# Kernel tuning notes

Hardware: AMD Instinct MI355X
Metric: run time of the kernel (lower is better)

Reference implementation:

```python
import jax, jax.numpy as jnp
import numpy as np
from jax.scipy.special import erf, erfinv

N_OBS = 8192   # number of observations
N_LOC = 2048   # number of spatial locations (q)


def setup_inputs() -> dict:
    key = jax.random.key(0)
    k1, k2, k3, k4 = jax.random.split(key, 4)
    # random 2-D coordinates -> symmetric pairwise squared-distance matrix (zero diag)
    coords = jax.random.uniform(k1, (N_LOC, 2), dtype=jnp.float32) * 10.0
    dist_matrix = jnp.sum((coords[:, None, :] - coords[None, :, :]) ** 2, axis=-1)  # [q,q]
    Z_idx = jax.random.randint(k2, (N_OBS,), 0, N_LOC)                              # location id per obs
    y_true = jax.random.normal(k3, (N_OBS, 1), dtype=jnp.float32)
    y_pred = jax.random.normal(k4, (N_OBS, 1), dtype=jnp.float32) * 0.5
    return {
        "y_true": y_true,
        "y_pred": y_pred,
        "Z_idx": Z_idx,
        "dist_matrix": dist_matrix,
        "sig2e": jnp.array([1.0], dtype=jnp.float32),
        "sig2bs": jnp.array([0.5], dtype=jnp.float32),
        "lengthscale": jnp.array([2.0], dtype=jnp.float32),
    }


def _inverse_gaussian_cdf(u):
    # tf.math.erfinv(2*clip(u,1e-5,1-1e-5)-1) * sqrt(2)
    return erfinv(2.0 * jnp.clip(u, 1e-5, 1.0 - 1e-5) - 1.0) * jnp.sqrt(2.0)


def reference(y_true, y_pred, Z_idx, dist_matrix, sig2e, sig2bs, lengthscale):
    N = y_true.shape[0]
    q = dist_matrix.shape[0]
    dt = y_true.dtype
    # getD: exponential distance kernel over locations  D = sig2b * exp(-M / (2*ell))
    D = sig2bs[0] * jnp.exp(-dist_matrix / (2.0 * lengthscale[0]))          # [q,q]
    # getZ: dense one-hot design matrix (sparse.to_dense of SparseTensor of ones)
    Z = jax.nn.one_hot(Z_idx, q, dtype=dt)                                   # [N,q]
    # V_batch: V = Z D Z' + sig2e * I
    V = Z @ (D @ Z.T) + sig2e[0] * jnp.eye(N, dtype=dt)                      # [N,N]
    sd = jnp.sqrt(jnp.diagonal(V))                                           # sd_sqrt_V
    R = V / (sd[:, None] * sd[None, :])                                      # correlation matrix
    # Gaussian marginal: sig2 = sig2e + sig2b (diag of V)
    sig2 = sig2e[0] + sig2bs[0]
    resid = y_true - y_pred                                                  # [N,1]
    # distribution.cdf_batch: standard normal CDF of resid / sqrt(sig2)
    u = 0.5 * (erf(resid / jnp.sqrt(2.0 * sig2)) + 1.0)
    m = _inverse_gaussian_cdf(u)                                             # [N,1]
    # distribution.sum_log_pdf_batch: sum of Gaussian log-pdf
    sum_log_pdf = jnp.sum(-0.5 * jnp.log(2.0 * jnp.pi * sig2) - resid ** 2 / (2.0 * sig2))
    # solve + logdet via a single Cholesky of the correlation matrix
    L = jnp.linalg.cholesky(R)
    V_inv_m = jax.scipy.linalg.cho_solve((L, True), m)                       # R^{-1} m
    logdet = 2.0 * jnp.sum(jnp.log(jnp.diagonal(L)))                         # logdet(V) - 2*sum(log sd)
    mV_invm = m.T @ V_inv_m                                                  # [1,1]
    mtm = m.T @ m                                                            # [1,1]
    total_loss = 0.5 * logdet + 0.5 * mV_invm - 0.5 * mtm + 0.5 * sum_log_pdf
    return total_loss  # [1,1]
```

## Files before the change

### kernel.cpp

```cpp
#include <hip/hip_runtime.h>
#include <math.h>

#define Q 2048
#define NOBS 8192

__device__ __forceinline__ float rl(float v, int l) {
  return __int_as_float(__builtin_amdgcn_readlane(__float_as_int(v), l));
}

__device__ __forceinline__ float block_sum256(float v, volatile float* red) {
  int tid = threadIdx.x;
#pragma unroll
  for (int o = 32; o > 0; o >>= 1) v += __shfl_down(v, o);
  __syncthreads();
  if ((tid & 63) == 0) red[tid >> 6] = v;
  __syncthreads();
  return red[0] + red[1] + red[2] + red[3];
}

__device__ __forceinline__ float chol64_reg(float rr[64], int lane) {
  float dv = 1.0f;
#pragma unroll
  for (int j = 0; j < 64; ++j) {
    float vjj = rl(rr[j], j);
    float invd = rsqrtf(vjj);
    float lij = rr[j] * invd;
    rr[j] = lij;
    if (lane == j) dv = lij;
#pragma unroll
    for (int k = j + 1; k < 64; ++k) rr[k] -= lij * rl(lij, k);
  }
  return dv;
}

__device__ __forceinline__ void wait_flag(int* f, int target) {
  while (__hip_atomic_load(f, __ATOMIC_RELAXED, __HIP_MEMORY_SCOPE_AGENT) <
         target)
    __builtin_amdgcn_s_sleep(8);
}

__global__ __launch_bounds__(256) void obs_kernel(
    const float* __restrict__ yt, const float* __restrict__ yp,
    const int* __restrict__ zidx, const float* __restrict__ s2e_p,
    const float* __restrict__ s2b_p, float* __restrict__ t,
    int* __restrict__ cnt, float* __restrict__ scal) {
  __shared__ float red[4];
  int i = blockIdx.x * 256 + threadIdx.x;
  float s2e = s2e_p[0], s2b = s2b_p[0];
  float sig2 = s2e + s2b;
  float r = yt[i] - yp[i];
  float e = erff(r * rsqrtf(2.0f * sig2));
  float u = 0.5f * (e + 1.0f);
  u = fminf(fmaxf(u, 1e-5f), 1.0f - 1e-5f);
  float m = erfinvf(2.0f * u - 1.0f) * 1.4142135623730951f;
  float slp = -0.5f * logf(2.0f * 3.14159265358979f * sig2) - r * r / (2.0f * sig2);
  int z = zidx[i];
  atomicAdd(&t[z], m);
  atomicAdd(&cnt[z], 1);
  float s1 = block_sum256(slp, red);
  float s2 = block_sum256(m * m, red);
  if (threadIdx.x == 0) {
    atomicAdd(&scal[0], s1);
    atomicAdd(&scal[1], s2);
  }
}

__global__ __launch_bounds__(256) void build_mv(
    const float* __restrict__ dist, const float* __restrict__ s2e_p,
    const float* __restrict__ s2b_p, const float* __restrict__ ell_p,
    const int* __restrict__ cnt, const float* __restrict__ t,
    float* __restrict__ G, float* __restrict__ z, float* __restrict__ scal) {
  __shared__ float red[4];
  int j = blockIdx.x;
  float s2e = s2e_p[0], s2b = s2b_p[0], ell = ell_p[0];
  float sig2 = s2e + s2b;
  float ratio = s2b / sig2;
  float diag = s2e / sig2;
  float inv2ell = 1.0f / (2.0f * ell);
  float cj = (float)cnt[j];
  const float* drow = dist + (size_t)j * Q;
  float* grow = G + (size_t)j * Q;
  float s = 0.0f;
  for (int k = threadIdx.x; k < Q; k += 256) {
    float e = expf(-drow[k] * inv2ell);
    s += e * t[k];
    float g = sqrtf(cj * (float)cnt[k]) * (ratio * e);
    if (j == k) g += diag;
    grow[k] = g;
  }
  float tot = block_sum256(s, red);
  if (threadIdx.x == 0) {
    float wj = ratio * tot;
    z[j] = sqrtf(cj) * wj;
    atomicAdd(&scal[2], t[j] * wj);
  }
}

__global__ __launch_bounds__(64, 1) void potrf_first(
    const float* __restrict__ G, float* __restrict__ dsA,
    float* __restrict__ z, float* __restrict__ scal) {
  int lane = threadIdx.x;
  float rr[64];
  const float* row = G + (size_t)lane * Q;
#pragma unroll
  for (int k4 = 0; k4 < 16; ++k4) {
    float4 v = *(const float4*)(row + k4 * 4);
    rr[k4 * 4 + 0] = v.x; rr[k4 * 4 + 1] = v.y;
    rr[k4 * 4 + 2] = v.z; rr[k4 * 4 + 3] = v.w;
  }
  float dv = chol64_reg(rr, lane);
#pragma unroll
  for (int k4 = 0; k4 < 16; ++k4) {
    float4 st;
    st.x = rr[k4 * 4 + 0]; st.y = rr[k4 * 4 + 1];
    st.z = rr[k4 * 4 + 2]; st.w = rr[k4 * 4 + 3];
    *(float4*)(dsA + lane * 64 + k4 * 4) = st;
  }
  float lg = logf(dv);
#pragma unroll
  for (int o = 32; o > 0; o >>= 1) lg += __shfl_down(lg, o);
  if (lane == 0) atomicAdd(&scal[3], lg);
  float a = z[lane];
  float myinv = 1.0f / dv;
#pragma unroll
  for (int p = 0; p < 64; ++p) {
    float xp = rl(a, p) * rl(myinv, p);
    if (lane > p) a -= xp * rr[p];
  }
  z[lane] = a * myinv;
}

__global__ __launch_bounds__(256, 2) void step_kernel(
    float* __restrict__ G, float* __restrict__ z, float* __restrict__ scal,
    const float* __restrict__ dsR, float* __restrict__ dsW,
    int* __restrict__ flags, int j0, int ntri, int n64, int T, int mode) {
  __shared__ __align__(16) float smem[2 * 64 * 68];
  __shared__ float z1s[64];
  __shared__ float z2s[64];
  float* shA = smem;
  float* shB = smem + 64 * 68;
  int tid = threadIdx.x, bx = blockIdx.x;
  int lane = tid & 63, wv = tid >> 6;
  int s1 = (j0 >> 6) + 1;
  int D0 = j0 + 64;
  int ztop = ntri + n64 - 1;

  if (mode == 1 || (mode == 0 && bx >= ztop)) {
    int t = (mode == 1) ? bx : bx - ztop;
#pragma unroll
    for (int it = 0; it < 4; ++it) {
      int idx = it * 256 + tid;
      int r = idx >> 4, c = (idx & 15) * 4;
      float4 v = *(const float4*)(dsR + r * 64 + c);
      shA[r * 65 + c + 0] = v.x; shA[r * 65 + c + 1] = v.y;
      shA[r * 65 + c + 2] = v.z; shA[r * 65 + c + 3] = v.w;
    }
    __syncthreads();
    int rbase = D0 + t * 16 + wv * 4;
    float* g0 = G + (size_t)(rbase + 0) * Q + j0;
    float* g1 = G + (size_t)(rbase + 1) * Q + j0;
    float* g2 = G + (size_t)(rbase + 2) * Q + j0;
    float* g3 = G + (size_t)(rbase + 3) * Q + j0;
    float a0 = g0[lane], a1 = g1[lane], a2 = g2[lane], a3 = g3[lane];
    float myinv = 1.0f / shA[lane * 65 + lane];
#pragma unroll
    for (int p = 0; p < 64; ++p) {
      float ip = rl(myinv, p);
      float x0 = rl(a0, p) * ip;
      float x1 = rl(a1, p) * ip;
      float x2 = rl(a2, p) * ip;
      float x3 = rl(a3, p) * ip;
      float lv = shA[lane * 65 + p];
      if (lane > p) {
        a0 -= x0 * lv; a1 -= x1 * lv; a2 -= x2 * lv; a3 -= x3 * lv;
      }
    }
    g0[lane] = a0 * myinv; g1[lane] = a1 * myinv;
    g2[lane] = a2 * myinv; g3[lane] = a3 * myinv;
    __syncthreads();
    if (tid == 0) {
      __builtin_amdgcn_fence(__ATOMIC_RELEASE, "agent");
      __hip_atomic_fetch_add(&flags[s1 + (t >> 2)], 1, __ATOMIC_RELAXED,
                             __HIP_MEMORY_SCOPE_AGENT);
    }
    return;
  }

  if (bx == 0) {
    if (tid == 0) {
      wait_flag(&flags[s1], T);
      __builtin_amdgcn_fence(__ATOMIC_ACQUIRE, "agent");
    }
    __syncthreads();
    if (tid < 64) z1s[tid] = z[j0 + tid];
#pragma unroll
    for (int it = 0; it < 4; ++it) {
      int idx = it * 256 + tid;
      int r2 = idx >> 4, c4 = (idx & 15) * 4;
      float4 v = *(const float4*)(G + (size_t)(D0 + r2) * Q + j0 + c4);
      shA[(c4 + 0) * 68 + r2] = v.x; shA[(c4 + 1) * 68 + r2] = v.y;
      shA[(c4 + 2) * 68 + r2] = v.z; shA[(c4 + 3) * 68 + r2] = v.w;
    }
    __syncthreads();
    int tx = tid & 15, ty = tid >> 4;
    float acc[4][4] = {{0.f}};
    for (int p = 0; p < 64; ++p) {
      float4 a4 = *(const float4*)&shA[p * 68 + ty * 4];
      float4 b4 = *(const float4*)&shA[p * 68 + tx * 4];
      float av[4] = {a4.x, a4.y, a4.z, a4.w};
      float bv[4] = {b4.x, b4.y, b4.z, b4.w};
#pragma unroll
      for (int i = 0; i < 4; ++i)
#pragma unroll
        for (int jj = 0; jj < 4; ++jj) acc[i][jj] += av[i] * bv[jj];
    }
    {
      int rw = tid >> 2, part = tid & 3;
      float ssum = 0.f;
      for (int p = part; p < 64; p += 4) ssum += shA[p * 68 + rw] * z1s[p];
      ssum += __shfl_down(ssum, 2);
      ssum += __shfl_down(ssum, 1);
      if (part == 0) z2s[rw] = z[D0 + rw] - ssum;
    }
#pragma unroll
    for (int i = 0; i < 4; ++i) {
      const float* gp = G + (size_t)(D0 + ty * 4 + i) * Q + D0 + tx * 4;
      float4 g = *(const float4*)gp;
      float4 o;
      o.x = g.x - acc[i][0]; o.y = g.y - acc[i][1];
      o.z = g.z - acc[i][2]; o.w = g.w - acc[i][3];
      *(float4*)&shB[(ty * 4 + i) * 68 + tx * 4] = o;
    }
    __syncthreads();
    if (tid < 64) {
      float rr[64];
#pragma unroll
      for (int k4 = 0; k4 < 16; ++k4) {
        float4 v = *(const float4*)&shB[lane * 68 + k4 * 4];
        rr[k4 * 4 + 0] = v.x; rr[k4 * 4 + 1] = v.y;
        rr[k4 * 4 + 2] = v.z; rr[k4 * 4 + 3] = v.w;
      }
      __builtin_amdgcn_s_setprio(1);
      float dv = chol64_reg(rr, lane);
      __builtin_amdgcn_s_setprio(0);
#pragma unroll
      for (int k4 = 0; k4 < 16; ++k4) {
        float4 st;
        st.x = rr[k4 * 4 + 0]; st.y = rr[k4 * 4 + 1];
        st.z = rr[k4 * 4 + 2]; st.w = rr[k4 * 4 + 3];
        *(float4*)(dsW + lane * 64 + k4 * 4) = st;
      }
      float lg = logf(dv);
#pragma unroll
      for (int o = 32; o > 0; o >>= 1) lg += __shfl_down(lg, o);
      if (lane == 0) atomicAdd(&scal[3], lg);
      float a = z2s[lane];
      float myinv = 1.0f / dv;
#pragma unroll
      for (int p = 0; p < 64; ++p) {
        float xp = rl(a, p) * rl(myinv, p);
        if (lane > p) a -= xp * rr[p];
      }
      z[D0 + lane] = a * myinv;
    }
    return;
  }

  if (bx < ntri) {
    int job = bx;
    int bi = (int)((sqrtf(8.0f * (float)job + 1.0f) - 1.0f) * 0.5f);
    while ((bi + 1) * (bi + 2) / 2 <= job) ++bi;
    while (bi * (bi + 1) / 2 > job) --bi;
    int bk = job - bi * (bi + 1) / 2;
    if (tid == 0) {
      wait_flag(&flags[s1 + bi], T);
      if (bk != bi) wait_flag(&flags[s1 + bk], T);
      __builtin_amdgcn_fence(__ATOMIC_ACQUIRE, "agent");
    }
    __syncthreads();
    int R0 = D0 + bi * 64, C0 = D0 + bk * 64;
    bool sym = (bi == bk);
#pragma unroll
    for (int it = 0; it < 4; ++it) {
      int idx = it * 256 + tid;
      int r = idx >> 4, c4 = (idx & 15) * 4;
      float4 v = *(const float4*)(G + (size_t)(R0 + r) * Q + j0 + c4);
      shA[(c4 + 0) * 68 + r] = v.x; shA[(c4 + 1) * 68 + r] = v.y;
      shA[(c4 + 2) * 68 + r] = v.z; shA[(c4 + 3) * 68 + r] = v.w;
      if (!sym) {
        float4 u = *(const float4*)(G + (size_t)(C0 + r) * Q + j0 + c4);
        shB[(c4 + 0) * 68 + r] = u.x; shB[(c4 + 1) * 68 + r] = u.y;
        shB[(c4 + 2) * 68 + r] = u.z; shB[(c4 + 3) * 68 + r] = u.w;
      }
    }
    __syncthreads();
    const float* sB = sym ? shA : shB;
    int tx = tid & 15, ty = tid >> 4;
    float acc[4][4] = {{0.f}};
    for (int p = 0; p < 64; ++p) {
      float4 a4 = *(const float4*)&shA[p * 68 + ty * 4];
      float4 b4 = *(const float4*)&sB[p * 68 + tx * 4];
      float av[4] = {a4.x, a4.y, a4.z, a4.w};
      float bv[4] = {b4.x, b4.y, b4.z, b4.w};
#pragma unroll
      for (int i = 0; i < 4; ++i)
#pragma unroll
        for (int jj = 0; jj < 4; ++jj) acc[i][jj] += av[i] * bv[jj];
    }
#pragma unroll
    for (int i = 0; i < 4; ++i) {
      float* gp = G + (size_t)(R0 + ty * 4 + i) * Q + C0 + tx * 4;
      float4 g = *(const float4*)gp;
      g.x -= acc[i][0]; g.y -= acc[i][1];
      g.z -= acc[i][2]; g.w -= acc[i][3];
      *(float4*)gp = g;
    }
    return;
  }

  {
    int bk = bx - ntri + 1;
    if (tid == 0) {
      wait_flag(&flags[s1 + bk], T);
      __builtin_amdgcn_fence(__ATOMIC_ACQUIRE, "agent");
    }
    __syncthreads();
    if (tid < 64) z1s[tid] = z[j0 + tid];
    __syncthreads();
    int C0 = D0 + bk * 64;
    int rw = tid >> 2, part = tid & 3;
    const float* Lr = G + (size_t)(C0 + rw) * Q + j0;
    float ssum = 0.f;
    for (int p = part; p < 64; p += 4) ssum += Lr[p] * z1s[p];
    ssum += __shfl_down(ssum, 2);
    ssum += __shfl_down(ssum, 1);
    if (part == 0) z[C0 + rw] -= ssum;
  }
}

__global__ __launch_bounds__(256) void final_assemble(
    const float* __restrict__ z, const float* __restrict__ scal,
    const float* __restrict__ s2e_p, const float* __restrict__ s2b_p,
    float* __restrict__ out) {
  __shared__ float red[4];
  int tid = threadIdx.x;
  float bv = 0.f;
  for (int i = tid; i < Q; i += 256) {
    float zi = z[i];
    bv += zi * zi;
  }
  float bvs = block_sum256(bv, red);
  if (tid == 0) {
    float s2e = s2e_p[0], s2b = s2b_p[0];
    float sig2 = s2e + s2b;
    float c = s2e / sig2;
    float slp = scal[0], mtm = scal[1];
    float tw = scal[2], sl = scal[3];
    float tty = (tw - bvs) / c;
    float mrm = (mtm - tty) / c;
    float logdetR = (float)(NOBS - Q) * logf(c) + 2.0f * sl;
    out[0] = 0.5f * logdetR + 0.5f * mrm - 0.5f * mtm + 0.5f * slp;
  }
}

extern "C" void kernel_launch(void* const* d_in, const int* in_sizes, int n_in,
                              void* d_out, int out_size, void* d_ws, size_t ws_size,
                              hipStream_t stream) {
  const float* yt   = (const float*)d_in[0];
  const float* yp   = (const float*)d_in[1];
  const int*   zidx = (const int*)d_in[2];
  const float* dist = (const float*)d_in[3];
  const float* s2e  = (const float*)d_in[4];
  const float* s2b  = (const float*)d_in[5];
  const float* ell  = (const float*)d_in[6];

  float* ws   = (float*)d_ws;
  float* G    = ws;
  float* z    = ws + (size_t)Q * Q;
  float* t    = z + Q;
  int*   cntv = (int*)(t + Q);
  float* scal = t + 2 * Q;
  int*   flags = (int*)(scal + 8);
  float* dsA  = scal + 8 + 64;
  float* dsB  = dsA + 4096;

  hipMemsetAsync(t, 0, (2 * Q + 8 + 64) * sizeof(float), stream);

  obs_kernel<<<NOBS / 256, 256, 0, stream>>>(yt, yp, zidx, s2e, s2b, t, cntv, scal);
  build_mv<<<Q, 256, 0, stream>>>(dist, s2e, s2b, ell, cntv, t, G, z, scal);

  potrf_first<<<1, 64, 0, stream>>>(G, dsA, z, scal);

  for (int s = 0; s < 31; ++s) {
    int n64 = 31 - s;
    int ntri = n64 * (n64 + 1) / 2;
    int j0 = s * 64;
    int T = 4 * (s + 1);
    float* dsR = (s & 1) ? dsB : dsA;
    float* dsW = (s & 1) ? dsA : dsB;
    int gfull = ntri + 5 * n64 - 1;
    if (gfull <= 512) {
      step_kernel<<<gfull, 256, 0, stream>>>(G, z, scal, dsR, dsW, flags,
                                             j0, ntri, n64, T, 0);
    } else {
      step_kernel<<<4 * n64, 256, 0, stream>>>(G, z, scal, dsR, dsW, flags,
                                               j0, ntri, n64, T, 1);
      step_kernel<<<ntri + n64 - 1, 256, 0, stream>>>(G, z, scal, dsR, dsW,
                                                      flags, j0, ntri, n64, T, 2);
    }
  }

  final_assemble<<<1, 256, 0, stream>>>(z, scal, s2e, s2b, (float*)d_out);
}
```

Baseline: 1.038 ms.

## Replace flag-synchronized Cholesky steps with redundant per-block panel factorization

Result: slower. 1.099 ms (+5.9%).

```diff
diff --git a/kernel.cpp b/kernel.cpp
--- a/kernel.cpp
+++ b/kernel.cpp
@@ -31,12 +31,6 @@
     for (int k = j + 1; k < 64; ++k) rr[k] -= lij * rl(lij, k);
   }
   return dv;
-}
-
-__device__ __forceinline__ void wait_flag(int* f, int target) {
-  while (__hip_atomic_load(f, __ATOMIC_RELAXED, __HIP_MEMORY_SCOPE_AGENT) <
-         target)
-    __builtin_amdgcn_s_sleep(8);
 }
 
 __global__ __launch_bounds__(256) void obs_kernel(
@@ -96,189 +90,178 @@
   }
 }
 
-__global__ __launch_bounds__(64, 1) void potrf_first(
-    const float* __restrict__ G, float* __restrict__ dsA,
-    float* __restrict__ z, float* __restrict__ scal) {
-  int lane = threadIdx.x;
-  float rr[64];
-  const float* row = G + (size_t)lane * Q;
-#pragma unroll
-  for (int k4 = 0; k4 < 16; ++k4) {
-    float4 v = *(const float4*)(row + k4 * 4);
-    rr[k4 * 4 + 0] = v.x; rr[k4 * 4 + 1] = v.y;
-    rr[k4 * 4 + 2] = v.z; rr[k4 * 4 + 3] = v.w;
-  }
-  float dv = chol64_reg(rr, lane);
-#pragma unroll
-  for (int k4 = 0; k4 < 16; ++k4) {
-    float4 st;
-    st.x = rr[k4 * 4 + 0]; st.y = rr[k4 * 4 + 1];
-    st.z = rr[k4 * 4 + 2]; st.w = rr[k4 * 4 + 3];
-    *(float4*)(dsA + lane * 64 + k4 * 4) = st;
-  }
-  float lg = logf(dv);
-#pragma unroll
-  for (int o = 32; o > 0; o >>= 1) lg += __shfl_down(lg, o);
-  if (lane == 0) atomicAdd(&scal[3], lg);
-  float a = z[lane];
-  float myinv = 1.0f / dv;
-#pragma unroll
-  for (int p = 0; p < 64; ++p) {
-    float xp = rl(a, p) * rl(myinv, p);
-    if (lane > p) a -= xp * rr[p];
-  }
-  z[lane] = a * myinv;
-}
-
-__global__ __launch_bounds__(256, 2) void step_kernel(
+__global__ __launch_bounds__(256, 1) void estep(
     float* __restrict__ G, float* __restrict__ z, float* __restrict__ scal,
-    const float* __restrict__ dsR, float* __restrict__ dsW,
-    int* __restrict__ flags, int j0, int ntri, int n64, int T, int mode) {
-  __shared__ __align__(16) float smem[2 * 64 * 68];
+    int j1, int m, int ntile) {
+  __shared__ __align__(16) float shA[64 * 68];
+  __shared__ __align__(16) float shB[64 * 68];
+  __shared__ __align__(16) float LT[64 * 64];
+  __shared__ float invDs[64];
   __shared__ float z1s[64];
   __shared__ float z2s[64];
-  float* shA = smem;
-  float* shB = smem + 64 * 68;
   int tid = threadIdx.x, bx = blockIdx.x;
-  int lane = tid & 63, wv = tid >> 6;
-  int s1 = (j0 >> 6) + 1;
-  int D0 = j0 + 64;
-  int ztop = ntri + n64 - 1;
-
-  if (mode == 1 || (mode == 0 && bx >= ztop)) {
-    int t = (mode == 1) ? bx : bx - ztop;
-#pragma unroll
-    for (int it = 0; it < 4; ++it) {
-      int idx = it * 256 + tid;
-      int r = idx >> 4, c = (idx & 15) * 4;
-      float4 v = *(const float4*)(dsR + r * 64 + c);
-      shA[r * 65 + c + 0] = v.x; shA[r * 65 + c + 1] = v.y;
-      shA[r * 65 + c + 2] = v.z; shA[r * 65 + c + 3] = v.w;
-    }
-    __syncthreads();
-    int rbase = D0 + t * 16 + wv * 4;
-    float* g0 = G + (size_t)(rbase + 0) * Q + j0;
-    float* g1 = G + (size_t)(rbase + 1) * Q + j0;
-    float* g2 = G + (size_t)(rbase + 2) * Q + j0;
-    float* g3 = G + (size_t)(rbase + 3) * Q + j0;
-    float a0 = g0[lane], a1 = g1[lane], a2 = g2[lane], a3 = g3[lane];
-    float myinv = 1.0f / shA[lane * 65 + lane];
-#pragma unroll
-    for (int p = 0; p < 64; ++p) {
-      float ip = rl(myinv, p);
-      float x0 = rl(a0, p) * ip;
-      float x1 = rl(a1, p) * ip;
-      float x2 = rl(a2, p) * ip;
-      float x3 = rl(a3, p) * ip;
-      float lv = shA[lane * 65 + p];
-      if (lane > p) {
-        a0 -= x0 * lv; a1 -= x1 * lv; a2 -= x2 * lv; a3 -= x3 * lv;
-      }
-    }
-    g0[lane] = a0 * myinv; g1[lane] = a1 * myinv;
-    g2[lane] = a2 * myinv; g3[lane] = a3 * myinv;
-    __syncthreads();
-    if (tid == 0) {
-      __builtin_amdgcn_fence(__ATOMIC_RELEASE, "agent");
-      __hip_atomic_fetch_add(&flags[s1 + (t >> 2)], 1, __ATOMIC_RELAXED,
-                             __HIP_MEMORY_SCOPE_AGENT);
-    }
-    return;
-  }
-
-  if (bx == 0) {
-    if (tid == 0) {
-      wait_flag(&flags[s1], T);
-      __builtin_amdgcn_fence(__ATOMIC_ACQUIRE, "agent");
-    }
-    __syncthreads();
-    if (tid < 64) z1s[tid] = z[j0 + tid];
-#pragma unroll
-    for (int it = 0; it < 4; ++it) {
-      int idx = it * 256 + tid;
-      int r2 = idx >> 4, c4 = (idx & 15) * 4;
-      float4 v = *(const float4*)(G + (size_t)(D0 + r2) * Q + j0 + c4);
-      shA[(c4 + 0) * 68 + r2] = v.x; shA[(c4 + 1) * 68 + r2] = v.y;
-      shA[(c4 + 2) * 68 + r2] = v.z; shA[(c4 + 3) * 68 + r2] = v.w;
-    }
-    __syncthreads();
-    int tx = tid & 15, ty = tid >> 4;
-    float acc[4][4] = {{0.f}};
-    for (int p = 0; p < 64; ++p) {
-      float4 a4 = *(const float4*)&shA[p * 68 + ty * 4];
-      float4 b4 = *(const float4*)&shA[p * 68 + tx * 4];
-      float av[4] = {a4.x, a4.y, a4.z, a4.w};
-      float bv[4] = {b4.x, b4.y, b4.z, b4.w};
-#pragma unroll
-      for (int i = 0; i < 4; ++i)
-#pragma unroll
-        for (int jj = 0; jj < 4; ++jj) acc[i][jj] += av[i] * bv[jj];
-    }
-    {
-      int rw = tid >> 2, part = tid & 3;
-      float ssum = 0.f;
-      for (int p = part; p < 64; p += 4) ssum += shA[p * 68 + rw] * z1s[p];
-      ssum += __shfl_down(ssum, 2);
-      ssum += __shfl_down(ssum, 1);
-      if (part == 0) z2s[rw] = z[D0 + rw] - ssum;
-    }
-#pragma unroll
-    for (int i = 0; i < 4; ++i) {
-      const float* gp = G + (size_t)(D0 + ty * 4 + i) * Q + D0 + tx * 4;
-      float4 g = *(const float4*)gp;
-      float4 o;
-      o.x = g.x - acc[i][0]; o.y = g.y - acc[i][1];
-      o.z = g.z - acc[i][2]; o.w = g.w - acc[i][3];
-      *(float4*)&shB[(ty * 4 + i) * 68 + tx * 4] = o;
-    }
-    __syncthreads();
+  int lane = tid & 63;
+  int j0 = j1 - 64;
+  int tx = tid & 15, ty = tid >> 4;
+
+  if (bx <= m) {
+    bool isdiag = (bx == 0);
+    int R0 = j1 + bx * 64;
+
+    if (j1 > 0) {
+#pragma unroll
+      for (int it = 0; it < 4; ++it) {
+        int idx = it * 256 + tid;
+        int r = idx >> 4, c4 = (idx & 15) * 4;
+        float4 v = *(const float4*)(G + (size_t)(j1 + r) * Q + j0 + c4);
+        shA[(c4 + 0) * 68 + r] = v.x; shA[(c4 + 1) * 68 + r] = v.y;
+        shA[(c4 + 2) * 68 + r] = v.z; shA[(c4 + 3) * 68 + r] = v.w;
+        if (!isdiag) {
+          float4 u = *(const float4*)(G + (size_t)(R0 + r) * Q + j0 + c4);
+          shB[(c4 + 0) * 68 + r] = u.x; shB[(c4 + 1) * 68 + r] = u.y;
+          shB[(c4 + 2) * 68 + r] = u.z; shB[(c4 + 3) * 68 + r] = u.w;
+        }
+      }
+      if (isdiag && tid < 64) z1s[tid] = z[j0 + tid];
+      __syncthreads();
+
+      float acc1[4][4] = {{0.f}};
+      float acc2[4][4] = {{0.f}};
+#pragma unroll 8
+      for (int p = 0; p < 64; ++p) {
+        float4 a4 = *(const float4*)&shA[p * 68 + ty * 4];
+        float4 b4 = *(const float4*)&shA[p * 68 + tx * 4];
+        float av[4] = {a4.x, a4.y, a4.z, a4.w};
+        float bv[4] = {b4.x, b4.y, b4.z, b4.w};
+#pragma unroll
+        for (int i = 0; i < 4; ++i)
+#pragma unroll
+          for (int jj = 0; jj < 4; ++jj) acc2[i][jj] += av[i] * bv[jj];
+        if (!isdiag) {
+          float4 c4v = *(const float4*)&shB[p * 68 + ty * 4];
+          float cv[4] = {c4v.x, c4v.y, c4v.z, c4v.w};
+#pragma unroll
+          for (int i = 0; i < 4; ++i)
+#pragma unroll
+            for (int jj = 0; jj < 4; ++jj) acc1[i][jj] += cv[i] * bv[jj];
+        }
+      }
+      if (isdiag) {
+        int rw = tid >> 2, part = tid & 3;
+        float ssum = 0.f;
+        for (int p = part; p < 64; p += 4) ssum += shA[p * 68 + rw] * z1s[p];
+        ssum += __shfl_down(ssum, 2);
+        ssum += __shfl_down(ssum, 1);
+        if (part == 0) z2s[rw] = z[j1 + rw] - ssum;
+      }
+      __syncthreads();
+
+#pragma unroll
+      for (int i = 0; i < 4; ++i) {
+        float4 g = *(const float4*)(G + (size_t)(j1 + ty * 4 + i) * Q + j1 + tx * 4);
+        shA[(ty * 4 + i) * 68 + tx * 4 + 0] = g.x - acc2[i][0];
+        shA[(ty * 4 + i) * 68 + tx * 4 + 1] = g.y - acc2[i][1];
+        shA[(ty * 4 + i) * 68 + tx * 4 + 2] = g.z - acc2[i][2];
+        shA[(ty * 4 + i) * 68 + tx * 4 + 3] = g.w - acc2[i][3];
+        if (!isdiag) {
+          float4 h = *(const float4*)(G + (size_t)(R0 + ty * 4 + i) * Q + j1 + tx * 4);
+          shB[(ty * 4 + i) * 68 + tx * 4 + 0] = h.x - acc1[i][0];
+          shB[(ty * 4 + i) * 68 + tx * 4 + 1] = h.y - acc1[i][1];
+          shB[(ty * 4 + i) * 68 + tx * 4 + 2] = h.z - acc1[i][2];
+          shB[(ty * 4 + i) * 68 + tx * 4 + 3] = h.w - acc1[i][3];
+        }
+      }
+      __syncthreads();
+    } else {
+#pragma unroll
+      for (int it = 0; it < 4; ++it) {
+        int idx = it * 256 + tid;
+        int r = idx >> 4, c4 = (idx & 15) * 4;
+        float4 g = *(const float4*)(G + (size_t)r * Q + c4);
+        shA[r * 68 + c4 + 0] = g.x; shA[r * 68 + c4 + 1] = g.y;
+        shA[r * 68 + c4 + 2] = g.z; shA[r * 68 + c4 + 3] = g.w;
+        if (!isdiag) {
+          float4 h = *(const float4*)(G + (size_t)(R0 + r) * Q + c4);
+          shB[r * 68 + c4 + 0] = h.x; shB[r * 68 + c4 + 1] = h.y;
+          shB[r * 68 + c4 + 2] = h.z; shB[r * 68 + c4 + 3] = h.w;
+        }
+      }
+      if (isdiag && tid < 64) z2s[tid] = z[tid];
+      __syncthreads();
+    }
+
     if (tid < 64) {
       float rr[64];
 #pragma unroll
       for (int k4 = 0; k4 < 16; ++k4) {
-        float4 v = *(const float4*)&shB[lane * 68 + k4 * 4];
+        float4 v = *(const float4*)&shA[lane * 68 + k4 * 4];
         rr[k4 * 4 + 0] = v.x; rr[k4 * 4 + 1] = v.y;
         rr[k4 * 4 + 2] = v.z; rr[k4 * 4 + 3] = v.w;
       }
       __builtin_amdgcn_s_setprio(1);
       float dv = chol64_reg(rr, lane);
       __builtin_amdgcn_s_setprio(0);
-#pragma unroll
-      for (int k4 = 0; k4 < 16; ++k4) {
-        float4 st;
-        st.x = rr[k4 * 4 + 0]; st.y = rr[k4 * 4 + 1];
-        st.z = rr[k4 * 4 + 2]; st.w = rr[k4 * 4 + 3];
-        *(float4*)(dsW + lane * 64 + k4 * 4) = st;
-      }
-      float lg = logf(dv);
-#pragma unroll
-      for (int o = 32; o > 0; o >>= 1) lg += __shfl_down(lg, o);
-      if (lane == 0) atomicAdd(&scal[3], lg);
-      float a = z2s[lane];
       float myinv = 1.0f / dv;
-#pragma unroll
-      for (int p = 0; p < 64; ++p) {
-        float xp = rl(a, p) * rl(myinv, p);
-        if (lane > p) a -= xp * rr[p];
-      }
-      z[D0 + lane] = a * myinv;
+      if (isdiag) {
+        float lg = logf(dv);
+#pragma unroll
+        for (int o = 32; o > 0; o >>= 1) lg += __shfl_down(lg, o);
+        if (lane == 0) atomicAdd(&scal[3], lg);
+        float a = z2s[lane];
+#pragma unroll
+        for (int p = 0; p < 64; ++p) {
+          float xp = rl(a, p) * rl(myinv, p);
+          if (lane > p) a -= xp * rr[p];
+        }
+        z[j1 + lane] = a * myinv;
+      } else {
+        invDs[lane] = myinv;
+#pragma unroll
+        for (int p = 0; p < 64; ++p)
+          LT[p * 64 + lane] = (p < lane) ? rr[p] : 0.0f;
+        float rr2[64];
+#pragma unroll
+        for (int k4 = 0; k4 < 16; ++k4) {
+          float4 v = *(const float4*)&shB[lane * 68 + k4 * 4];
+          rr2[k4 * 4 + 0] = v.x; rr2[k4 * 4 + 1] = v.y;
+          rr2[k4 * 4 + 2] = v.z; rr2[k4 * 4 + 3] = v.w;
+        }
+        __builtin_amdgcn_s_setprio(1);
+#pragma unroll
+        for (int p = 0; p < 64; ++p) {
+          float xp = rr2[p] * invDs[p];
+          rr2[p] = xp;
+#pragma unroll
+          for (int k4 = 0; k4 < 16; ++k4) {
+            if (k4 * 4 + 3 > p) {
+              float4 l4 = *(const float4*)&LT[p * 64 + k4 * 4];
+              rr2[k4 * 4 + 0] -= xp * l4.x;
+              rr2[k4 * 4 + 1] -= xp * l4.y;
+              rr2[k4 * 4 + 2] -= xp * l4.z;
+              rr2[k4 * 4 + 3] -= xp * l4.w;
+            }
+          }
+        }
+        __builtin_amdgcn_s_setprio(0);
+#pragma unroll
+        for (int k4 = 0; k4 < 16; ++k4) {
+          float4 st;
+          st.x = rr2[k4 * 4 + 0]; st.y = rr2[k4 * 4 + 1];
+          st.z = rr2[k4 * 4 + 2]; st.w = rr2[k4 * 4 + 3];
+          *(float4*)(G + (size_t)(R0 + lane) * Q + j1 + k4 * 4) = st;
+        }
+      }
     }
     return;
   }
 
-  if (bx < ntri) {
-    int job = bx;
-    int bi = (int)((sqrtf(8.0f * (float)job + 1.0f) - 1.0f) * 0.5f);
-    while ((bi + 1) * (bi + 2) / 2 <= job) ++bi;
-    while (bi * (bi + 1) / 2 > job) --bi;
-    int bk = job - bi * (bi + 1) / 2;
-    if (tid == 0) {
-      wait_flag(&flags[s1 + bi], T);
-      if (bk != bi) wait_flag(&flags[s1 + bk], T);
-      __builtin_amdgcn_fence(__ATOMIC_ACQUIRE, "agent");
-    }
-    __syncthreads();
-    int R0 = D0 + bi * 64, C0 = D0 + bk * 64;
+  int tjob = bx - (m + 1);
+  if (tjob < ntile) {
+    int bi = (int)((sqrtf(8.0f * (float)tjob + 1.0f) - 1.0f) * 0.5f);
+    while ((bi + 1) * (bi + 2) / 2 <= tjob) ++bi;
+    while (bi * (bi + 1) / 2 > tjob) --bi;
+    int bk = tjob - bi * (bi + 1) / 2;
+    int R0 = j1 + 64 + bi * 64, C0 = j1 + 64 + bk * 64;
     bool sym = (bi == bk);
 #pragma unroll
     for (int it = 0; it < 4; ++it) {
@@ -295,8 +278,8 @@
     }
     __syncthreads();
     const float* sB = sym ? shA : shB;
-    int tx = tid & 15, ty = tid >> 4;
     float acc[4][4] = {{0.f}};
+#pragma unroll 8
     for (int p = 0; p < 64; ++p) {
       float4 a4 = *(const float4*)&shA[p * 68 + ty * 4];
       float4 b4 = *(const float4*)&sB[p * 68 + tx * 4];
@@ -319,22 +302,17 @@
   }
 
   {
-    int bk = bx - ntri + 1;
-    if (tid == 0) {
-      wait_flag(&flags[s1 + bk], T);
-      __builtin_amdgcn_fence(__ATOMIC_ACQUIRE, "agent");
-    }
-    __syncthreads();
+    int zb = tjob - ntile;
+    int B0 = j1 + 64 + zb * 64;
     if (tid < 64) z1s[tid] = z[j0 + tid];
     __syncthreads();
-    int C0 = D0 + bk * 64;
     int rw = tid >> 2, part = tid & 3;
-    const float* Lr = G + (size_t)(C0 + rw) * Q + j0;
+    const float* Lr = G + (size_t)(B0 + rw) * Q + j0;
     float ssum = 0.f;
     for (int p = part; p < 64; p += 4) ssum += Lr[p] * z1s[p];
     ssum += __shfl_down(ssum, 2);
     ssum += __shfl_down(ssum, 1);
-    if (part == 0) z[C0 + rw] -= ssum;
+    if (part == 0) z[B0 + rw] -= ssum;
   }
 }
 
@@ -380,34 +358,19 @@
   float* t    = z + Q;
   int*   cntv = (int*)(t + Q);
   float* scal = t + 2 * Q;
-  int*   flags = (int*)(scal + 8);
-  float* dsA  = scal + 8 + 64;
-  float* dsB  = dsA + 4096;
-
-  hipMemsetAsync(t, 0, (2 * Q + 8 + 64) * sizeof(float), stream);
+
+  hipMemsetAsync(t, 0, (2 * Q + 8) * sizeof(float), stream);
 
   obs_kernel<<<NOBS / 256, 256, 0, stream>>>(yt, yp, zidx, s2e, s2b, t, cntv, scal);
   build_mv<<<Q, 256, 0, stream>>>(dist, s2e, s2b, ell, cntv, t, G, z, scal);
 
-  potrf_first<<<1, 64, 0, stream>>>(G, dsA, z, scal);
-
-  for (int s = 0; s < 31; ++s) {
-    int n64 = 31 - s;
-    int ntri = n64 * (n64 + 1) / 2;
-    int j0 = s * 64;
-    int T = 4 * (s + 1);
-    float* dsR = (s & 1) ? dsB : dsA;
-    float* dsW = (s & 1) ? dsA : dsB;
-    int gfull = ntri + 5 * n64 - 1;
-    if (gfull <= 512) {
-      step_kernel<<<gfull, 256, 0, stream>>>(G, z, scal, dsR, dsW, flags,
-                                             j0, ntri, n64, T, 0);
-    } else {
-      step_kernel<<<4 * n64, 256, 0, stream>>>(G, z, scal, dsR, dsW, flags,
-                                               j0, ntri, n64, T, 1);
-      step_kernel<<<ntri + n64 - 1, 256, 0, stream>>>(G, z, scal, dsR, dsW,
-                                                      flags, j0, ntri, n64, T, 2);
-    }
+  estep<<<32, 256, 0, stream>>>(G, z, scal, 0, 31, 0);
+
+  for (int s = 0; s <= 30; ++s) {
+    int j1 = (s + 1) * 64;
+    int m = 30 - s;
+    int ntile = m * (m + 1) / 2;
+    estep<<<1 + 2 * m + ntile, 256, 0, stream>>>(G, z, scal, j1, m, ntile);
   }
 
   final_assemble<<<1, 256, 0, stream>>>(z, scal, s2e, s2b, (float*)d_out);
```
